# Optimization experiments

Measured on AMD Instinct MI355X. Metric: run time of the kernel, lower is better.

Reference implementation:

```python
import jax, jax.numpy as jnp
import numpy as np


def _c1(x, W, b):
    # 1x1 conv: W [out,in], x [B,in,H,W]
    return jnp.einsum('oi,bihw->bohw', W, x) + b[None, :, None, None]


def _c3(x, W, b):
    # 3x3 conv, stride 1, padding 1 (SAME)
    y = jax.lax.conv_general_dilated(x, W, (1, 1), 'SAME',
                                     dimension_numbers=('NCHW', 'OIHW', 'NCHW'))
    return y + b[None, :, None, None]


def _resize(x, h, w):
    # matches torch F.interpolate(mode='bilinear', align_corners=False)
    return jax.image.resize(x, (x.shape[0], x.shape[1], h, w), 'linear', antialias=False)


def setup_inputs() -> dict:
    key = jax.random.key(0)
    ks = jax.random.split(key, 20)
    B, C, H, W = 4, 64, 128, 128
    d = C // 8

    def n(k, shape, s=0.05):
        return jax.random.normal(k, shape, dtype=jnp.float32) * s

    z = lambda c: jnp.zeros((c,), jnp.float32)
    return {
        'x': jax.random.normal(ks[0], (B, C, H, W), dtype=jnp.float32),
        'mask': jax.random.normal(ks[1], (B, 64, H, W), dtype=jnp.float32),
        'Wq': n(ks[2], (d, C)), 'bq': z(d),
        'Wk': n(ks[3], (d, C)), 'bk': z(d),
        'Wv': n(ks[4], (C, C)), 'bv': z(C),
        'alpha1': jax.random.uniform(ks[5], (1,), dtype=jnp.float32),
        'alpha2': jax.random.uniform(ks[6], (1,), dtype=jnp.float32),
        'mq_w1': n(ks[7], (64, 64, 3, 3)), 'mq_b1': z(64),
        'mq_w2': n(ks[8], (d, 64)), 'mq_b2': z(d),
        'mk_w1': n(ks[9], (64, 64, 3, 3)), 'mk_b1': z(64),
        'mk_w2': n(ks[10], (d, 64)), 'mk_b2': z(d),
        'ca_w1': n(ks[11], (64, 64)), 'ca_b1': z(64),
        'ca_w2': n(ks[12], (64, 64)), 'ca_b2': z(64),
    }


def reference(x, mask, Wq, bq, Wk, bk, Wv, bv, alpha1, alpha2,
              mq_w1, mq_b1, mq_w2, mq_b2, mk_w1, mk_b1, mk_w2, mk_b2,
              ca_w1, ca_b1, ca_w2, ca_b2):
    B, C, H, W = x.shape
    h2, w2 = H // 2, W // 2
    N = h2 * w2

    mask_q = _c1(jax.nn.relu(_c3(mask, mq_w1, mq_b1)), mq_w2, mq_b2)
    mask_k = _c1(jax.nn.relu(_c3(mask, mk_w1, mk_b1)), mk_w2, mk_b2)
    xq = _c1(x, Wq, bq)  # [B, d, H, W]
    xk = _c1(x, Wk, bk)

    pq = mask_q * xq * alpha1 + xq * (1.0 - alpha1)
    pq = _resize(pq, h2, w2).reshape(B, -1, N)          # [B, d, N]
    pk = mask_k * xk * alpha2 + xk * (1.0 - alpha2)
    pk = _resize(pk, h2, w2).reshape(B, -1, N)          # [B, d, N]

    energy = jnp.einsum('bdn,bdm->bnm', pq, pk)         # [B, N, N]
    attn = jax.nn.softmax(energy, axis=-1)

    pv = _resize(_c1(x, Wv, bv), h2, w2).reshape(B, C, N)
    out = jnp.einsum('bcn,bmn->bcm', pv, attn)          # value @ attn^T
    out = out.reshape(B, C, h2, w2)
    out = _resize(out, H, W)
    out = _c1(jax.nn.relu(_c1(out, ca_w1, ca_b1)), ca_w2, ca_b2)
    return out + x
```

## Files before the change

kernel.cpp:

```cpp
#include <hip/hip_runtime.h>
#include <hip/hip_bf16.h>

typedef _Float16 half8 __attribute__((ext_vector_type(8)));
typedef _Float16 half4v __attribute__((ext_vector_type(4)));
typedef _Float16 half2v __attribute__((ext_vector_type(2)));
typedef __fp16 pkh2 __attribute__((ext_vector_type(2)));
typedef float f32x4 __attribute__((ext_vector_type(4)));

static __device__ __forceinline__ f32x4 mfma16(half8 a, half8 b, f32x4 c) {
    return __builtin_amdgcn_mfma_f32_16x16x32_f16(a, b, c, 0, 0, 0);
}

typedef const __attribute__((address_space(1))) unsigned int* gas_ptr;
typedef __attribute__((address_space(3))) unsigned int* las_ptr;
static __device__ __forceinline__ void gload16(const void* g, void* l) {
    __builtin_amdgcn_global_load_lds((gas_ptr)g, (las_ptr)l, 16, 0, 0);
}

static __device__ __forceinline__ half2v cvt2(float a, float b) {
    pkh2 t = __builtin_amdgcn_cvt_pkrtz(a, b);
    return __builtin_bit_cast(half2v, t);
}
static __device__ __forceinline__ half8 pk8(f32x4 a, f32x4 b) {
    half2v x0 = cvt2(a[0], a[1]);
    half2v x1 = cvt2(a[2], a[3]);
    half2v x2 = cvt2(b[0], b[1]);
    half2v x3 = cvt2(b[2], b[3]);
    half4v lo = __builtin_shufflevector(x0, x1, 0, 1, 2, 3);
    half4v hi = __builtin_shufflevector(x2, x3, 0, 1, 2, 3);
    return __builtin_shufflevector(lo, hi, 0, 1, 2, 3, 4, 5, 6, 7);
}
static __device__ __forceinline__ half4v pk4(f32x4 a) {
    half2v x0 = cvt2(a[0], a[1]);
    half2v x1 = cvt2(a[2], a[3]);
    return __builtin_shufflevector(x0, x1, 0, 1, 2, 3);
}

#define WS_APCONV   0u
#define WS_APW2S    147456u
#define WS_APCA     151552u
#define WS_APW2K4   159744u
#define WS_PACKED   196608u
#define WS_MASKQ    8849408u
#define WS_MASKK    10946560u
#define WS_Q16      13043712u
#define WS_K16      13305856u
#define WS_V16      13568000u
#define WS_ZB       15665152u
#define WS_PACC8    17762304u
#define WS_PML8     34539520u
#define WS_END8     35063808u
#define WS_PACC4    WS_PACKED
#define WS_PML4     WS_MASKQ

__global__ __launch_bounds__(256) void prep_pack_kernel(
    const float* __restrict__ mask,
    const float* __restrict__ mqw1, const float* __restrict__ mkw1,
    const float* __restrict__ mqw2, const float* __restrict__ mkw2,
    const float* __restrict__ caw1, const float* __restrict__ caw2,
    _Float16* __restrict__ packed,
    _Float16* __restrict__ ApackConv, _Float16* __restrict__ ApackW2s,
    _Float16* __restrict__ ApackCA, _Float16* __restrict__ ApackW2K4)
{
    int tid = threadIdx.x;
    if (blockIdx.z < 4) {
        int ich = blockIdx.y, b = blockIdx.z;
        _Float16* Pb = packed + ((size_t)b * 8 + ich) * 130 * 130 * 8;
        if (blockIdx.x < 2) {
            for (int p = blockIdx.x * 260 + tid; p < (int)(blockIdx.x + 1) * 260; p += 256) {
                int row, col;
                if (p < 130)      { row = 0;       col = p; }
                else if (p < 260) { row = 129;     col = p - 130; }
                else if (p < 390) { row = p - 260; col = 0; }
                else              { row = p - 390; col = 129; }
                half8 z = {};
                *(half8*)(Pb + ((size_t)row * 130 + col) * 8) = z;
            }
        }
        int x = tid & 127;
        int sy = blockIdx.x * 2 + (tid >> 7);
        half8 v;
#pragma unroll
        for (int cc = 0; cc < 8; cc++)
            v[cc] = (_Float16)mask[(((size_t)(b * 64 + ich * 8 + cc)) * 128 + sy) * 128 + x];
        *(half8*)(Pb + (((size_t)(sy + 1)) * 130 + (x + 1)) * 8) = v;
        return;
    }
    int tid0 = (blockIdx.y * 64 + blockIdx.x) * 256 + tid;
    const int stride = 512 * 256;
    for (int idx = tid0; idx < 73728; idx += stride) {
        int j = idx & 7, lane = (idx >> 3) & 63, mf = (idx >> 9) & 3;
        int ks18 = idx >> 11;
        int br = ks18 / 18, kstep = ks18 % 18;
        int oc = mf * 16 + (lane & 15);
        int g = lane >> 4;
        int k = kstep * 32 + g * 8 + j;
        int tap = k >> 6, ic = k & 63;
        int dy = tap / 3, dx = tap - dy * 3;
        const float* w1 = br ? mkw1 : mqw1;
        ApackConv[idx] = (_Float16)w1[((oc * 64 + ic) * 3 + dy) * 3 + dx];
    }
    for (int idx = tid0; idx < 2048; idx += stride) {
        int j = idx & 7, lane = (idx >> 3) & 63;
        int f = (idx >> 9) & 1, br = idx >> 10;
        int dc = lane & 15, g = lane >> 4;
        int kap = 16 * (2 * f + (j >> 2)) + 4 * g + (j & 3);
        const float* w2 = br ? mkw2 : mqw2;
        ApackW2s[idx] = (_Float16)((dc < 8) ? w2[dc * 64 + kap] : 0.f);
    }
    for (int idx = tid0; idx < 4096; idx += stride) {
        int j = idx & 7, lane = (idx >> 3) & 63, mf = (idx >> 9) & 3, f = idx >> 11;
        int cp = mf * 16 + (lane & 15), g = lane >> 4;
        int kap = 16 * (2 * f + (j >> 2)) + 4 * g + (j & 3);
        ApackCA[idx] = (_Float16)caw1[cp * 64 + kap];
    }
    for (int idx = tid0; idx < 4096; idx += stride) {
        int j = idx & 7, lane = (idx >> 3) & 63, mf = (idx >> 9) & 3, f = idx >> 11;
        int cc = mf * 16 + (lane & 15), g = lane >> 4;
        int cpk = f * 32 + g * 8 + j;
        ApackW2K4[idx] = (_Float16)caw2[cc * 64 + cpk];
    }
}

__global__ __launch_bounds__(256) void conv_mask_kernel(
    const _Float16* __restrict__ packed,
    const _Float16* __restrict__ ApackConv,
    const _Float16* __restrict__ ApackW2s,
    const float* __restrict__ mqb1, const float* __restrict__ mqb2,
    const float* __restrict__ mkb1, const float* __restrict__ mkb2,
    _Float16* __restrict__ maskq, _Float16* __restrict__ maskk)
{
    __shared__ __align__(16) _Float16 S[8 * 4 * 72 * 8];
    int tid = threadIdx.x;
    int lane = tid & 63, w = tid >> 6;
    int x0 = blockIdx.x * 64;
    int y0 = blockIdx.y * 2;
    int b = blockIdx.z;
    int row = w & 1, br = w >> 1;
    int q = lane & 15, g = lane >> 4;

    const _Float16* Pb = packed + (size_t)b * 8 * 130 * 130 * 8;
#pragma unroll
    for (int i = 0; i < 8; i++) {
        int p = w * 8 + i;
        int ich = p >> 2, pr = p & 3;
        const _Float16* src = Pb + (((size_t)ich * 130 + (y0 + pr)) * 130 + x0) * 8;
        _Float16* dst = S + ((ich * 4 + pr) * 72) * 8;
        gload16(src + lane * 8, dst);
        if (lane < 8) gload16(src + (64 + lane) * 8, dst + 64 * 8);
    }
    __syncthreads();

    const _Float16* Ab = ApackConv + br * 36864;
    f32x4 acc[4][4] = {};
    for (int kstep = 0; kstep < 18; kstep++) {
        int tap = kstep >> 1;
        int dyv = tap / 3, dxv = tap - dyv * 3;
        int ich = (kstep & 1) * 4 + g;
        const _Float16* srow = S + ((ich * 4 + row + dyv) * 72 + q + dxv) * 8;
        half8 bf[4];
#pragma unroll
        for (int nf = 0; nf < 4; nf++)
            bf[nf] = *(const half8*)(srow + nf * 128);
        const _Float16* Ak = Ab + kstep * 2048 + lane * 8;
#pragma unroll
        for (int mf = 0; mf < 4; mf++) {
            half8 af = *(const half8*)(Ak + mf * 512);
#pragma unroll
            for (int nf = 0; nf < 4; nf++)
                acc[mf][nf] = mfma16(af, bf[nf], acc[mf][nf]);
        }
    }
    const float* b1p = br ? mkb1 : mqb1;
    const float* b2p = br ? mkb2 : mqb2;
    _Float16* outp = br ? maskk : maskq;
    float b1v[16];
#pragma unroll
    for (int mf = 0; mf < 4; mf++)
#pragma unroll
        for (int r = 0; r < 4; r++) b1v[mf * 4 + r] = b1p[mf * 16 + g * 4 + r];
    f32x4 acc2[4] = {};
#pragma unroll
    for (int f = 0; f < 2; f++) {
        half8 a2 = *(const half8*)(ApackW2s + (br * 2 + f) * 512 + lane * 8);
#pragma unroll
        for (int nf = 0; nf < 4; nf++) {
            half8 b2f;
#pragma unroll
            for (int j = 0; j < 8; j++) {
                int mfj = 2 * f + (j >> 2), rj = j & 3;
                b2f[j] = (_Float16)fmaxf(acc[mfj][nf][rj] + b1v[mfj * 4 + rj], 0.f);
            }
            acc2[nf] = mfma16(a2, b2f, acc2[nf]);
        }
    }
    if (g < 2) {
        int y = y0 + row;
#pragma unroll
        for (int r = 0; r < 4; r++) {
            int dc = g * 4 + r;
            float bb = b2p[dc];
#pragma unroll
            for (int nf = 0; nf < 4; nf++)
                outp[((size_t)(b * 8 + dc) * 128 + y) * 128 + (x0 + nf * 16 + q)] =
                    (_Float16)(acc2[nf][r] + bb);
        }
    }
}

__global__ __launch_bounds__(512) void proj_kernel(
    const float* __restrict__ xg,
    const _Float16* __restrict__ maskq, const _Float16* __restrict__ maskk,
    const float* __restrict__ Wq, const float* __restrict__ bq,
    const float* __restrict__ Wk, const float* __restrict__ bk,
    const float* __restrict__ Wv, const float* __restrict__ bv,
    const float* __restrict__ a1p, const float* __restrict__ a2p,
    _Float16* __restrict__ Qg, _Float16* __restrict__ Kg, _Float16* __restrict__ Vg)
{
    __shared__ float xr[16384];
    __shared__ float xw[4096];
    __shared__ float lWv[4096], lWq[512], lWk[512];
    int tid = threadIdx.x;
    int b = blockIdx.x >> 6, i = blockIdx.x & 63;

    for (int idx = tid; idx < 16384; idx += 512) {
        int ic = idx >> 8, rem = idx & 255;
        xr[idx] = xg[((size_t)(b * 64 + ic) * 128 + (2 * i + (rem >> 7))) * 128 + (rem & 127)];
    }
    for (int idx = tid; idx < 4096; idx += 512) lWv[idx] = Wv[idx];
    lWq[tid] = Wq[tid];
    lWk[tid] = Wk[tid];
    __syncthreads();
    for (int idx = tid; idx < 4096; idx += 512) {
        int ic = idx >> 6, j = idx & 63;
        const float* base = &xr[ic * 256 + 2 * j];
        xw[idx] = 0.25f * (base[0] + base[1] + base[128] + base[129]);
    }
    __syncthreads();

    if (tid < 256) {
        int c0 = tid >> 5;
        int j0 = (tid & 31) * 2;
        float acc0[8], acc1[8];
#pragma unroll
        for (int u = 0; u < 8; u++) { float bb = bv[c0 + 8 * u]; acc0[u] = bb; acc1[u] = bb; }
        for (int ic = 0; ic < 64; ic++) {
            float x0v = xw[ic * 64 + j0], x1v = xw[ic * 64 + j0 + 1];
#pragma unroll
            for (int u = 0; u < 8; u++) {
                float ww = lWv[(c0 + 8 * u) * 64 + ic];
                acc0[u] += ww * x0v; acc1[u] += ww * x1v;
            }
        }
        int f = j0 >> 5, gg = (j0 & 15) >> 2, hi = (j0 >> 4) & 1;
        int off = (f * 4 + gg) * 8 + (j0 & 3) + 4 * hi;
#pragma unroll
        for (int u = 0; u < 8; u++) {
            int c = c0 + 8 * u;
            _Float16* p = Vg + (size_t)(b * 64 + c) * 4096 + i * 64 + off;
            p[0] = (_Float16)acc0[u]; p[1] = (_Float16)acc1[u];
        }
    } else {
        int t = tid - 256;
        int branch = t >> 7;
        int ysel = t & 1;
        int j = (t >> 1) & 63;
        const float* W = branch ? lWk : lWq;
        const float* bias = branch ? bk : bq;
        float alpha = branch ? a2p[0] : a1p[0];
        const _Float16* mq = branch ? maskk : maskq;
        _Float16* outg = branch ? Kg : Qg;
        int x0c = 2 * j, x1c = 2 * j + 1;
        float aq0[8], aq1[8];
#pragma unroll
        for (int dc = 0; dc < 8; dc++) { float bb = bias[dc]; aq0[dc] = bb; aq1[dc] = bb; }
        for (int ic = 0; ic < 64; ic++) {
            float xv0 = xr[ic * 256 + ysel * 128 + x0c];
            float xv1 = xr[ic * 256 + ysel * 128 + x1c];
#pragma unroll
            for (int dc = 0; dc < 8; dc++) {
                float ww = W[dc * 64 + ic];
                aq0[dc] += ww * xv0; aq1[dc] += ww * xv1;
            }
        }
        int yy = 2 * i + ysel;
        half8 vq;
#pragma unroll
        for (int dc = 0; dc < 8; dc++) {
            size_t mbase = ((size_t)(b * 8 + dc) * 128 + yy) * 128;
            float m0v = (float)mq[mbase + x0c], m1v = (float)mq[mbase + x1c];
            float s = aq0[dc] * (alpha * m0v + (1.f - alpha))
                    + aq1[dc] * (alpha * m1v + (1.f - alpha));
            s += __shfl_xor(s, 1);
            vq[dc] = (_Float16)(0.25f * s);
        }
        if (ysel == 0)
            *(half8*)(outg + ((size_t)b * 4096 + i * 64 + j) * 8) = vq;
    }
}

__global__ __launch_bounds__(512, 4) void attn_kernel(
    const _Float16* __restrict__ Qg, const _Float16* __restrict__ Kg,
    const _Float16* __restrict__ Vg, const _Float16* __restrict__ ApackCA,
    _Float16* __restrict__ pacc, float* __restrict__ pml,
    int bmask, int sshift, int bbase)
{
    __shared__ __align__(16) _Float16 Vlds[8 * 4096];
    __shared__ __align__(16) _Float16 Klds[8 * 512];
    int tid = threadIdx.x, lane = tid & 63, w = tid >> 6;
    int q = lane & 15, g = lane >> 4;
    int bid = blockIdx.x;
    int qt = bid & 31, b = bbase + ((bid >> 5) & bmask), s = bid >> sshift;

    const _Float16* Kb = Kg + ((size_t)b * 4096 + s * 512) * 8;
    const _Float16* Vbase = Vg + (size_t)b * 64 * 4096 + s * 512;

    {
        int cc = w * 8 + (lane >> 3);
        int chl = (lane & 7) ^ (cc & 7);
        const _Float16* src0 = Vbase + (size_t)cc * 4096 + chl * 8;
#pragma unroll
        for (int t = 0; t < 8; t++)
            gload16(src0 + t * 64, Vlds + t * 4096 + w * 512);
        gload16(Kb + (size_t)(w * 64 + lane) * 8, Klds + w * 512);
    }
    half8 qf = {};
    if (g == 0) {
        int qb = qt * 128 + w * 16 + q;
        half8 r0 = *(const half8*)(Qg + ((size_t)b * 4096 + qb) * 8);
#pragma unroll
        for (int j = 0; j < 8; j++)
            qf[j] = (_Float16)((float)r0[j] * 1.44269504f);
    }
    __syncthreads();

    half8 ones;
#pragma unroll
    for (int j = 0; j < 8; j++) ones[j] = (_Float16)1.f;

    f32x4 acc[4] = {};
    f32x4 accl = {};
    const f32x4 zero4 = {};

#pragma unroll 1
    for (int t = 0; t < 8; t++) {
        const _Float16* Kt = Klds + t * 512;
        half8 af0 = *(const half8*)(Kt + q * 8);
        half8 af1 = *(const half8*)(Kt + (16 + q) * 8);
        half8 af2 = *(const half8*)(Kt + (32 + q) * 8);
        half8 af3 = *(const half8*)(Kt + (48 + q) * 8);

        f32x4 s0 = mfma16(af0, qf, zero4);
        f32x4 s1 = mfma16(af1, qf, zero4);
        f32x4 s2 = mfma16(af2, qf, zero4);
        f32x4 s3 = mfma16(af3, qf, zero4);
        f32x4 e0, e1, e2, e3;
#pragma unroll
        for (int r = 0; r < 4; r++) {
            e0[r] = __builtin_amdgcn_exp2f(s0[r]);
            e1[r] = __builtin_amdgcn_exp2f(s1[r]);
            e2[r] = __builtin_amdgcn_exp2f(s2[r]);
            e3[r] = __builtin_amdgcn_exp2f(s3[r]);
        }
        half8 pb0 = pk8(e0, e1), pb1 = pk8(e2, e3);
        accl = mfma16(ones, pb0, accl);
        accl = mfma16(ones, pb1, accl);

        const _Float16* Vl = Vlds + t * 4096;
        int sw = q & 7;
        __builtin_amdgcn_s_setprio(1);
#pragma unroll
        for (int mfc = 0; mfc < 4; mfc++) {
            const _Float16* vr = Vl + (mfc * 16 + q) * 64;
            half8 av0 = *(const half8*)(vr + (g ^ sw) * 8);
            half8 av1 = *(const half8*)(vr + ((4 + g) ^ sw) * 8);
            acc[mfc] = mfma16(av0, pb0, acc[mfc]);
            acc[mfc] = mfma16(av1, pb1, acc[mfc]);
        }
        __builtin_amdgcn_s_setprio(0);
    }

    half8 ob0 = pk8(acc[0], acc[1]);
    half8 ob1 = pk8(acc[2], acc[3]);
    f32x4 z[4] = {};
#pragma unroll
    for (int mf2 = 0; mf2 < 4; mf2++) {
        half8 a30 = *(const half8*)(ApackCA + mf2 * 512 + lane * 8);
        half8 a31 = *(const half8*)(ApackCA + (4 + mf2) * 512 + lane * 8);
        z[mf2] = mfma16(a30, ob0, z[mf2]);
        z[mf2] = mfma16(a31, ob1, z[mf2]);
    }
    size_t prow = ((size_t)bid * 128 + w * 16 + q) * 64;
#pragma unroll
    for (int mf2 = 0; mf2 < 4; mf2++)
        *(half4v*)(pacc + prow + mf2 * 16 + g * 4) = pk4(z[mf2]);
    if (g == 0) pml[bid * 128 + w * 16 + q] = accl[0];
}

__global__ __launch_bounds__(256) void combine_kernel(
    const _Float16* __restrict__ pacc, const float* __restrict__ pml,
    const float* __restrict__ cb1, _Float16* __restrict__ zb,
    int tps, int bbase)
{
    int T = blockIdx.x * 256 + threadIdx.x;
    int e = T & 7, row = T >> 3;
    int brel = row >> 12, qg = row & 4095;
    int qt = qg >> 7, ql = qg & 127;
    int tb0 = brel * 32 + qt;

    float sum[8] = {};
    float L = 0.f;
    for (int s = 0; s < 8; s++) {
        int tile = s * tps + tb0;
        half8 v = *(const half8*)(pacc + ((size_t)tile * 128 + ql) * 64 + e * 8);
#pragma unroll
        for (int i = 0; i < 8; i++) sum[i] += (float)v[i];
        L += pml[tile * 128 + ql];
    }
    float inv = 1.f / L;
    half8 o;
#pragma unroll
    for (int i = 0; i < 8; i++) o[i] = (_Float16)(sum[i] * inv + cb1[e * 8 + i]);
    *(half8*)(zb + ((size_t)(bbase + brel) * 4096 + qg) * 64 + e * 8) = o;
}

__global__ __launch_bounds__(512) void post_kernel(
    const _Float16* __restrict__ zg,
    const float* __restrict__ xg,
    const _Float16* __restrict__ ApackW2K4, const float* __restrict__ cb2,
    float* __restrict__ outg)
{
    __shared__ _Float16 zt[6 * 18 * 72];
    int tid = threadIdx.x, lane = tid & 63, w = tid >> 6;
    int x0 = blockIdx.x * 32, y0 = blockIdx.y * 8, b = blockIdx.z;
    int r0 = 4 * (int)blockIdx.y - 1;
    int cbs = 16 * (int)blockIdx.x - 1;
    const _Float16* zgb = zg + (size_t)b * 4096 * 64;
    for (int idx = tid; idx < 864; idx += 512) {
        int rowi = idx >> 3, ch = idx & 7;
        int r = rowi / 18, col = rowi - r * 18;
        int zr = min(max(r0 + r, 0), 63);
        int zc = min(max(cbs + col, 0), 63);
        half8 v = *(const half8*)(zgb + ((size_t)(zr * 64 + zc)) * 64 + ch * 8);
        *(half8*)&zt[(r * 18 + col) * 72 + ch * 8] = v;
    }
    __syncthreads();

    int q = lane & 15, g = lane >> 4;
    int y = y0 + w;
    int ra = (w >> 1) + (w & 1);
    float wyA = (w & 1) ? 0.75f : 0.25f;
    float wyB = 1.f - wyA;
    f32x4 acc[4][2] = {};
#pragma unroll
    for (int f = 0; f < 2; f++) {
        half8 a[4];
#pragma unroll
        for (int mf = 0; mf < 4; mf++)
            a[mf] = *(const half8*)(ApackW2K4 + (f * 4 + mf) * 512 + lane * 8);
#pragma unroll
        for (int nf = 0; nf < 2; nf++) {
            int pxl = nf * 16 + q;
            int ca = (pxl >> 1) + (pxl & 1);
            float wxA = (pxl & 1) ? 0.75f : 0.25f;
            float wxB = 1.f - wxA;
            half8 bfrag;
#pragma unroll
            for (int qd = 0; qd < 2; qd++) {
                int cpb = f * 32 + g * 8 + qd * 4;
                const _Float16* z00 = &zt[(ra * 18 + ca) * 72 + cpb];
                half4v h00 = *(const half4v*)z00;
                half4v h01 = *(const half4v*)(z00 + 72);
                half4v h10 = *(const half4v*)(z00 + 18 * 72);
                half4v h11 = *(const half4v*)(z00 + 18 * 72 + 72);
#pragma unroll
                for (int e = 0; e < 4; e++) {
                    float zu = ((float)h00[e] * wxA + (float)h01[e] * wxB) * wyA
                             + ((float)h10[e] * wxA + (float)h11[e] * wxB) * wyB;
                    bfrag[qd * 4 + e] = (_Float16)fmaxf(zu, 0.f);
                }
            }
#pragma unroll
            for (int mf = 0; mf < 4; mf++) acc[mf][nf] = mfma16(a[mf], bfrag, acc[mf][nf]);
        }
    }
#pragma unroll
    for (int mf = 0; mf < 4; mf++)
#pragma unroll
        for (int r = 0; r < 4; r++) {
            int c = mf * 16 + g * 4 + r;
            float bb = cb2[c];
#pragma unroll
            for (int nf = 0; nf < 2; nf++) {
                size_t oidx = ((size_t)(b * 64 + c) * 128 + y) * 128 + x0 + nf * 16 + q;
                outg[oidx] = acc[mf][nf][r] + bb + xg[oidx];
            }
        }
}

extern "C" void kernel_launch(void* const* d_in, const int* in_sizes, int n_in,
                              void* d_out, int out_size, void* d_ws, size_t ws_size,
                              hipStream_t stream)
{
    const float* x    = (const float*)d_in[0];
    const float* mask = (const float*)d_in[1];
    const float* Wq   = (const float*)d_in[2];
    const float* bq   = (const float*)d_in[3];
    const float* Wk   = (const float*)d_in[4];
    const float* bk   = (const float*)d_in[5];
    const float* Wv   = (const float*)d_in[6];
    const float* bv   = (const float*)d_in[7];
    const float* a1   = (const float*)d_in[8];
    const float* a2   = (const float*)d_in[9];
    const float* mqw1 = (const float*)d_in[10];
    const float* mqb1 = (const float*)d_in[11];
    const float* mqw2 = (const float*)d_in[12];
    const float* mqb2 = (const float*)d_in[13];
    const float* mkw1 = (const float*)d_in[14];
    const float* mkb1 = (const float*)d_in[15];
    const float* mkw2 = (const float*)d_in[16];
    const float* mkb2 = (const float*)d_in[17];
    const float* caw1 = (const float*)d_in[18];
    const float* cab1 = (const float*)d_in[19];
    const float* caw2 = (const float*)d_in[20];
    const float* cab2 = (const float*)d_in[21];

    char* ws = (char*)d_ws;
    _Float16* ApackConv = (_Float16*)(ws + WS_APCONV);
    _Float16* ApackW2s  = (_Float16*)(ws + WS_APW2S);
    _Float16* ApackCA   = (_Float16*)(ws + WS_APCA);
    _Float16* ApackW2K4 = (_Float16*)(ws + WS_APW2K4);
    _Float16* packed    = (_Float16*)(ws + WS_PACKED);
    _Float16* maskq     = (_Float16*)(ws + WS_MASKQ);
    _Float16* maskk     = (_Float16*)(ws + WS_MASKK);
    _Float16* Qg16      = (_Float16*)(ws + WS_Q16);
    _Float16* Kg16      = (_Float16*)(ws + WS_K16);
    _Float16* Vb        = (_Float16*)(ws + WS_V16);
    _Float16* zb        = (_Float16*)(ws + WS_ZB);

    prep_pack_kernel<<<dim3(64, 8, 5), dim3(256), 0, stream>>>(
        mask, mqw1, mkw1, mqw2, mkw2, caw1, caw2,
        packed, ApackConv, ApackW2s, ApackCA, ApackW2K4);
    conv_mask_kernel<<<dim3(2, 64, 4), dim3(256), 0, stream>>>(
        packed, ApackConv, ApackW2s, mqb1, mqb2, mkb1, mkb2, maskq, maskk);
    proj_kernel<<<dim3(256), dim3(512), 0, stream>>>(
        x, maskq, maskk, Wq, bq, Wk, bk, Wv, bv, a1, a2, Qg16, Kg16, Vb);

    bool big = (ws_size >= (size_t)WS_END8);
    if (big) {
        _Float16* pacc = (_Float16*)(ws + WS_PACC8);
        float*    pml  = (float*)(ws + WS_PML8);
        attn_kernel<<<dim3(1024), dim3(512), 0, stream>>>(
            Qg16, Kg16, Vb, ApackCA, pacc, pml, 3, 7, 0);
        combine_kernel<<<dim3(512), dim3(256), 0, stream>>>(pacc, pml, cab1, zb, 128, 0);
    } else {
        _Float16* pacc = (_Float16*)(ws + WS_PACC4);
        float*    pml  = (float*)(ws + WS_PML4);
        for (int bbase = 0; bbase < 4; bbase += 2) {
            attn_kernel<<<dim3(512), dim3(512), 0, stream>>>(
                Qg16, Kg16, Vb, ApackCA, pacc, pml, 1, 6, bbase);
            combine_kernel<<<dim3(256), dim3(256), 0, stream>>>(pacc, pml, cab1, zb, 64, bbase);
        }
    }
    post_kernel<<<dim3(4, 16, 4), dim3(512), 0, stream>>>(
        zb, x, ApackW2K4, cab2, (float*)d_out);
}
```

Before: 80.61 us.

## Move V projection into prep kernel, fuse combine into post, retile mask conv

Computes the pooled V projection in extra blocks of the prep kernel and splits the old proj kernel into a lighter QK-only kernel that keeps x in fp16 shared memory. The mask conv now stages its packed weights in LDS and handles four rows per block with one branch per block, and the attention tile loop is unrolled by two. In the big-workspace path the split-softmax combine is folded into the post kernel, which removes a kernel launch and the zb round trip. The cost is that the post kernel recomputes combined values for halo pixels, and the prep kernel now uses more shared memory.

```diff
diff --git a/kernel.cpp b/kernel.cpp
--- a/kernel.cpp
+++ b/kernel.cpp
@@ -58,10 +58,14 @@
     const float* __restrict__ mqw1, const float* __restrict__ mkw1,
     const float* __restrict__ mqw2, const float* __restrict__ mkw2,
     const float* __restrict__ caw1, const float* __restrict__ caw2,
+    const float* __restrict__ xg,
+    const float* __restrict__ Wv, const float* __restrict__ bv,
     _Float16* __restrict__ packed,
     _Float16* __restrict__ ApackConv, _Float16* __restrict__ ApackW2s,
-    _Float16* __restrict__ ApackCA, _Float16* __restrict__ ApackW2K4)
+    _Float16* __restrict__ ApackCA, _Float16* __restrict__ ApackW2K4,
+    _Float16* __restrict__ Vg)
 {
+    __shared__ float vshm[6144];
     int tid = threadIdx.x;
     if (blockIdx.z < 4) {
         int ich = blockIdx.y, b = blockIdx.z;
@@ -86,6 +90,51 @@
         *(half8*)(Pb + (((size_t)(sy + 1)) * 130 + (x + 1)) * 8) = v;
         return;
     }
+    if (blockIdx.z == 5) {
+        int vb = blockIdx.y * 64 + blockIdx.x;
+        if (vb >= 256) return;
+        float* xw = vshm;
+        float* lWv = vshm + 2048;
+        int b = vb >> 6, i = vb & 63;
+        for (int idx = tid; idx < 2048; idx += 256) {
+            int ic = idx >> 5, j = idx & 31;
+            const float* px = xg + ((size_t)(b * 64 + ic) * 128 + 2 * i) * 128 + 2 * j;
+            xw[idx] = 0.25f * (px[0] + px[1] + px[128] + px[129]);
+        }
+        for (int idx = tid; idx < 4096; idx += 256) lWv[idx] = Wv[idx];
+        __syncthreads();
+        for (int jh = 0; jh < 2; jh++) {
+            if (jh == 1) {
+                __syncthreads();
+                for (int idx = tid; idx < 2048; idx += 256) {
+                    int ic = idx >> 5, j = idx & 31;
+                    const float* px = xg + ((size_t)(b * 64 + ic) * 128 + 2 * i) * 128 + 2 * (32 + j);
+                    xw[idx] = 0.25f * (px[0] + px[1] + px[128] + px[129]);
+                }
+                __syncthreads();
+            }
+            int c0 = tid >> 5;
+            int jl = tid & 31;
+            float acc0[8];
+#pragma unroll
+            for (int u = 0; u < 8; u++) acc0[u] = bv[c0 + 8 * u];
+            for (int ic = 0; ic < 64; ic++) {
+                float xv = xw[ic * 32 + jl];
+#pragma unroll
+                for (int u = 0; u < 8; u++)
+                    acc0[u] += lWv[(c0 + 8 * u) * 64 + ic] * xv;
+            }
+            int j0 = jh * 32 + jl;
+            int f = j0 >> 5, gg = (j0 & 15) >> 2, hi = (j0 >> 4) & 1;
+            int off = (f * 4 + gg) * 8 + (j0 & 3) + 4 * hi;
+#pragma unroll
+            for (int u = 0; u < 8; u++) {
+                int c = c0 + 8 * u;
+                Vg[(size_t)(b * 64 + c) * 4096 + i * 64 + off] = (_Float16)acc0[u];
+            }
+        }
+        return;
+    }
     int tid0 = (blockIdx.y * 64 + blockIdx.x) * 256 + tid;
     const int stride = 512 * 256;
     for (int idx = tid0; idx < 73728; idx += stride) {
@@ -130,39 +179,46 @@
     const float* __restrict__ mkb1, const float* __restrict__ mkb2,
     _Float16* __restrict__ maskq, _Float16* __restrict__ maskk)
 {
-    __shared__ __align__(16) _Float16 S[8 * 4 * 72 * 8];
+    __shared__ __align__(16) _Float16 A[36864];
+    __shared__ __align__(16) _Float16 S[28032];
     int tid = threadIdx.x;
     int lane = tid & 63, w = tid >> 6;
     int x0 = blockIdx.x * 64;
-    int y0 = blockIdx.y * 2;
-    int b = blockIdx.z;
-    int row = w & 1, br = w >> 1;
+    int y0 = blockIdx.y * 4;
+    int bz = blockIdx.z;
+    int b = bz >> 1, br = bz & 1;
     int q = lane & 15, g = lane >> 4;
 
+    const _Float16* Ag = ApackConv + br * 36864;
+#pragma unroll
+    for (int i = 0; i < 18; i++) {
+        int off = w * 9216 + i * 512;
+        gload16(Ag + off + lane * 8, A + off);
+    }
     const _Float16* Pb = packed + (size_t)b * 8 * 130 * 130 * 8;
 #pragma unroll
-    for (int i = 0; i < 8; i++) {
-        int p = w * 8 + i;
-        int ich = p >> 2, pr = p & 3;
+    for (int i = 0; i < 12; i++) {
+        int rr = w * 12 + i;
+        int ich = rr / 6, pr = rr - ich * 6;
         const _Float16* src = Pb + (((size_t)ich * 130 + (y0 + pr)) * 130 + x0) * 8;
-        _Float16* dst = S + ((ich * 4 + pr) * 72) * 8;
+        _Float16* dst = S + (ich * 6 + pr) * 584;
         gload16(src + lane * 8, dst);
-        if (lane < 8) gload16(src + (64 + lane) * 8, dst + 64 * 8);
+        if (lane < 8) gload16(src + (64 + lane) * 8, dst + 512);
     }
     __syncthreads();
 
-    const _Float16* Ab = ApackConv + br * 36864;
     f32x4 acc[4][4] = {};
+#pragma unroll
     for (int kstep = 0; kstep < 18; kstep++) {
         int tap = kstep >> 1;
         int dyv = tap / 3, dxv = tap - dyv * 3;
         int ich = (kstep & 1) * 4 + g;
-        const _Float16* srow = S + ((ich * 4 + row + dyv) * 72 + q + dxv) * 8;
+        const _Float16* srow = S + ((ich * 6 + w + dyv) * 73 + q + dxv) * 8;
         half8 bf[4];
 #pragma unroll
         for (int nf = 0; nf < 4; nf++)
             bf[nf] = *(const half8*)(srow + nf * 128);
-        const _Float16* Ak = Ab + kstep * 2048 + lane * 8;
+        const _Float16* Ak = A + kstep * 2048 + lane * 8;
 #pragma unroll
         for (int mf = 0; mf < 4; mf++) {
             half8 af = *(const half8*)(Ak + mf * 512);
@@ -195,7 +251,7 @@
         }
     }
     if (g < 2) {
-        int y = y0 + row;
+        int y = y0 + w;
 #pragma unroll
         for (int r = 0; r < 4; r++) {
             int dc = g * 4 + r;
@@ -208,95 +264,64 @@
     }
 }
 
-__global__ __launch_bounds__(512) void proj_kernel(
+__global__ __launch_bounds__(256) void qkproj_kernel(
     const float* __restrict__ xg,
     const _Float16* __restrict__ maskq, const _Float16* __restrict__ maskk,
     const float* __restrict__ Wq, const float* __restrict__ bq,
     const float* __restrict__ Wk, const float* __restrict__ bk,
-    const float* __restrict__ Wv, const float* __restrict__ bv,
     const float* __restrict__ a1p, const float* __restrict__ a2p,
-    _Float16* __restrict__ Qg, _Float16* __restrict__ Kg, _Float16* __restrict__ Vg)
+    _Float16* __restrict__ Qg, _Float16* __restrict__ Kg)
 {
-    __shared__ float xr[16384];
-    __shared__ float xw[4096];
-    __shared__ float lWv[4096], lWq[512], lWk[512];
+    __shared__ _Float16 xr[16384];
+    __shared__ float lWq[512], lWk[512];
     int tid = threadIdx.x;
     int b = blockIdx.x >> 6, i = blockIdx.x & 63;
 
-    for (int idx = tid; idx < 16384; idx += 512) {
+    for (int idx = tid; idx < 16384; idx += 256) {
         int ic = idx >> 8, rem = idx & 255;
-        xr[idx] = xg[((size_t)(b * 64 + ic) * 128 + (2 * i + (rem >> 7))) * 128 + (rem & 127)];
-    }
-    for (int idx = tid; idx < 4096; idx += 512) lWv[idx] = Wv[idx];
+        xr[idx] = (_Float16)xg[((size_t)(b * 64 + ic) * 128 + (2 * i + (rem >> 7))) * 128 + (rem & 127)];
+    }
     lWq[tid] = Wq[tid];
+    lWq[tid + 256] = Wq[tid + 256];
     lWk[tid] = Wk[tid];
+    lWk[tid + 256] = Wk[tid + 256];
     __syncthreads();
-    for (int idx = tid; idx < 4096; idx += 512) {
-        int ic = idx >> 6, j = idx & 63;
-        const float* base = &xr[ic * 256 + 2 * j];
-        xw[idx] = 0.25f * (base[0] + base[1] + base[128] + base[129]);
-    }
-    __syncthreads();
-
-    if (tid < 256) {
-        int c0 = tid >> 5;
-        int j0 = (tid & 31) * 2;
-        float acc0[8], acc1[8];
-#pragma unroll
-        for (int u = 0; u < 8; u++) { float bb = bv[c0 + 8 * u]; acc0[u] = bb; acc1[u] = bb; }
-        for (int ic = 0; ic < 64; ic++) {
-            float x0v = xw[ic * 64 + j0], x1v = xw[ic * 64 + j0 + 1];
-#pragma unroll
-            for (int u = 0; u < 8; u++) {
-                float ww = lWv[(c0 + 8 * u) * 64 + ic];
-                acc0[u] += ww * x0v; acc1[u] += ww * x1v;
-            }
-        }
-        int f = j0 >> 5, gg = (j0 & 15) >> 2, hi = (j0 >> 4) & 1;
-        int off = (f * 4 + gg) * 8 + (j0 & 3) + 4 * hi;
-#pragma unroll
-        for (int u = 0; u < 8; u++) {
-            int c = c0 + 8 * u;
-            _Float16* p = Vg + (size_t)(b * 64 + c) * 4096 + i * 64 + off;
-            p[0] = (_Float16)acc0[u]; p[1] = (_Float16)acc1[u];
-        }
-    } else {
-        int t = tid - 256;
-        int branch = t >> 7;
-        int ysel = t & 1;
-        int j = (t >> 1) & 63;
-        const float* W = branch ? lWk : lWq;
-        const float* bias = branch ? bk : bq;
-        float alpha = branch ? a2p[0] : a1p[0];
-        const _Float16* mq = branch ? maskk : maskq;
-        _Float16* outg = branch ? Kg : Qg;
-        int x0c = 2 * j, x1c = 2 * j + 1;
-        float aq0[8], aq1[8];
-#pragma unroll
-        for (int dc = 0; dc < 8; dc++) { float bb = bias[dc]; aq0[dc] = bb; aq1[dc] = bb; }
-        for (int ic = 0; ic < 64; ic++) {
-            float xv0 = xr[ic * 256 + ysel * 128 + x0c];
-            float xv1 = xr[ic * 256 + ysel * 128 + x1c];
-#pragma unroll
-            for (int dc = 0; dc < 8; dc++) {
-                float ww = W[dc * 64 + ic];
-                aq0[dc] += ww * xv0; aq1[dc] += ww * xv1;
-            }
-        }
-        int yy = 2 * i + ysel;
-        half8 vq;
+
+    int branch = tid >> 7;
+    int t = tid & 127;
+    int ysel = t & 1;
+    int j = (t >> 1) & 63;
+    const float* W = branch ? lWk : lWq;
+    const float* bias = branch ? bk : bq;
+    float alpha = branch ? a2p[0] : a1p[0];
+    const _Float16* mq = branch ? maskk : maskq;
+    _Float16* outg = branch ? Kg : Qg;
+    int x0c = 2 * j, x1c = 2 * j + 1;
+    float aq0[8], aq1[8];
+#pragma unroll
+    for (int dc = 0; dc < 8; dc++) { float bb = bias[dc]; aq0[dc] = bb; aq1[dc] = bb; }
+    for (int ic = 0; ic < 64; ic++) {
+        float xv0 = (float)xr[ic * 256 + ysel * 128 + x0c];
+        float xv1 = (float)xr[ic * 256 + ysel * 128 + x1c];
 #pragma unroll
         for (int dc = 0; dc < 8; dc++) {
-            size_t mbase = ((size_t)(b * 8 + dc) * 128 + yy) * 128;
-            float m0v = (float)mq[mbase + x0c], m1v = (float)mq[mbase + x1c];
-            float s = aq0[dc] * (alpha * m0v + (1.f - alpha))
-                    + aq1[dc] * (alpha * m1v + (1.f - alpha));
-            s += __shfl_xor(s, 1);
-            vq[dc] = (_Float16)(0.25f * s);
-        }
-        if (ysel == 0)
-            *(half8*)(outg + ((size_t)b * 4096 + i * 64 + j) * 8) = vq;
-    }
+            float ww = W[dc * 64 + ic];
+            aq0[dc] += ww * xv0; aq1[dc] += ww * xv1;
+        }
+    }
+    int yy = 2 * i + ysel;
+    half8 vq;
+#pragma unroll
+    for (int dc = 0; dc < 8; dc++) {
+        size_t mbase = ((size_t)(b * 8 + dc) * 128 + yy) * 128;
+        float m0v = (float)mq[mbase + x0c], m1v = (float)mq[mbase + x1c];
+        float s = aq0[dc] * (alpha * m0v + (1.f - alpha))
+                + aq1[dc] * (alpha * m1v + (1.f - alpha));
+        s += __shfl_xor(s, 1);
+        vq[dc] = (_Float16)(0.25f * s);
+    }
+    if (ysel == 0)
+        *(half8*)(outg + ((size_t)b * 4096 + i * 64 + j) * 8) = vq;
 }
 
 __global__ __launch_bounds__(512, 4) void attn_kernel(
@@ -342,7 +367,7 @@
     f32x4 accl = {};
     const f32x4 zero4 = {};
 
-#pragma unroll 1
+#pragma unroll 2
     for (int t = 0; t < 8; t++) {
         const _Float16* Kt = Klds + t * 512;
         half8 af0 = *(const half8*)(Kt + q * 8);
@@ -424,8 +449,11 @@
     *(half8*)(zb + ((size_t)(bbase + brel) * 4096 + qg) * 64 + e * 8) = o;
 }
 
+template <int FUSED>
 __global__ __launch_bounds__(512) void post_kernel(
     const _Float16* __restrict__ zg,
+    const _Float16* __restrict__ pacc, const float* __restrict__ pml,
+    const float* __restrict__ cb1,
     const float* __restrict__ xg,
     const _Float16* __restrict__ ApackW2K4, const float* __restrict__ cb2,
     float* __restrict__ outg)
@@ -441,8 +469,29 @@
         int r = rowi / 18, col = rowi - r * 18;
         int zr = min(max(r0 + r, 0), 63);
         int zc = min(max(cbs + col, 0), 63);
-        half8 v = *(const half8*)(zgb + ((size_t)(zr * 64 + zc)) * 64 + ch * 8);
-        *(half8*)&zt[(r * 18 + col) * 72 + ch * 8] = v;
+        if constexpr (FUSED) {
+            int zq = zr * 64 + zc;
+            int tb = b * 32 + (zq >> 7);
+            int ql = zq & 127;
+            float sum[8] = {};
+            float L = 0.f;
+#pragma unroll
+            for (int s = 0; s < 8; s++) {
+                int tile = s * 128 + tb;
+                half8 v = *(const half8*)(pacc + ((size_t)tile * 128 + ql) * 64 + ch * 8);
+#pragma unroll
+                for (int i2 = 0; i2 < 8; i2++) sum[i2] += (float)v[i2];
+                L += pml[tile * 128 + ql];
+            }
+            float inv = 1.f / L;
+            half8 o;
+#pragma unroll
+            for (int i2 = 0; i2 < 8; i2++) o[i2] = (_Float16)(sum[i2] * inv + cb1[ch * 8 + i2]);
+            *(half8*)&zt[(r * 18 + col) * 72 + ch * 8] = o;
+        } else {
+            half8 v = *(const half8*)(zgb + ((size_t)(zr * 64 + zc)) * 64 + ch * 8);
+            *(half8*)&zt[(r * 18 + col) * 72 + ch * 8] = v;
+        }
     }
     __syncthreads();
 
@@ -538,13 +587,13 @@
     _Float16* Vb        = (_Float16*)(ws + WS_V16);
     _Float16* zb        = (_Float16*)(ws + WS_ZB);
 
-    prep_pack_kernel<<<dim3(64, 8, 5), dim3(256), 0, stream>>>(
-        mask, mqw1, mkw1, mqw2, mkw2, caw1, caw2,
-        packed, ApackConv, ApackW2s, ApackCA, ApackW2K4);
-    conv_mask_kernel<<<dim3(2, 64, 4), dim3(256), 0, stream>>>(
+    prep_pack_kernel<<<dim3(64, 8, 6), dim3(256), 0, stream>>>(
+        mask, mqw1, mkw1, mqw2, mkw2, caw1, caw2, x, Wv, bv,
+        packed, ApackConv, ApackW2s, ApackCA, ApackW2K4, Vb);
+    conv_mask_kernel<<<dim3(2, 32, 8), dim3(256), 0, stream>>>(
         packed, ApackConv, ApackW2s, mqb1, mqb2, mkb1, mkb2, maskq, maskk);
-    proj_kernel<<<dim3(256), dim3(512), 0, stream>>>(
-        x, maskq, maskk, Wq, bq, Wk, bk, Wv, bv, a1, a2, Qg16, Kg16, Vb);
+    qkproj_kernel<<<dim3(256), dim3(256), 0, stream>>>(
+        x, maskq, maskk, Wq, bq, Wk, bk, a1, a2, Qg16, Kg16);
 
     bool big = (ws_size >= (size_t)WS_END8);
     if (big) {
@@ -552,7 +601,8 @@
         float*    pml  = (float*)(ws + WS_PML8);
         attn_kernel<<<dim3(1024), dim3(512), 0, stream>>>(
             Qg16, Kg16, Vb, ApackCA, pacc, pml, 3, 7, 0);
-        combine_kernel<<<dim3(512), dim3(256), 0, stream>>>(pacc, pml, cab1, zb, 128, 0);
+        post_kernel<1><<<dim3(4, 16, 4), dim3(512), 0, stream>>>(
+            zb, pacc, pml, cab1, x, ApackW2K4, cab2, (float*)d_out);
     } else {
         _Float16* pacc = (_Float16*)(ws + WS_PACC4);
         float*    pml  = (float*)(ws + WS_PML4);
@@ -561,7 +611,7 @@
                 Qg16, Kg16, Vb, ApackCA, pacc, pml, 1, 6, bbase);
             combine_kernel<<<dim3(256), dim3(256), 0, stream>>>(pacc, pml, cab1, zb, 64, bbase);
         }
-    }
-    post_kernel<<<dim3(4, 16, 4), dim3(512), 0, stream>>>(
-        zb, x, ApackW2K4, cab2, (float*)d_out);
-}
+        post_kernel<0><<<dim3(4, 16, 4), dim3(512), 0, stream>>>(
+            zb, nullptr, nullptr, cab1, x, ApackW2K4, cab2, (float*)d_out);
+    }
+}
```

Result: faster. 78.59 us (-2.5%).
